# Optimization experiments

Measured on AMD Instinct MI355X. Metric: run time of the kernel, lower is better.

## Reference

```python
import jax, jax.numpy as jnp
import numpy as np

N_NODES = 50000
N_EDGES = 600000
HID = 128
N_CONVS = 3
N_GRAPHS = 64


def setup_inputs() -> dict:
    key = jax.random.key(0)
    ks = jax.random.split(key, 8)
    scale = 1.0 / np.sqrt(HID)  # ~xavier
    node_attr = jax.random.normal(ks[0], (N_NODES, HID), dtype=jnp.float32)
    edge_attr = jax.random.normal(ks[1], (N_EDGES, HID), dtype=jnp.float32)
    edge_index = jax.random.randint(ks[2], (2, N_EDGES), 0, N_NODES, dtype=jnp.int32)
    batch = jnp.sort(jax.random.randint(ks[3], (N_NODES,), 0, N_GRAPHS, dtype=jnp.int32))
    W1 = jax.random.normal(ks[4], (N_CONVS, HID, HID), dtype=jnp.float32) * scale
    B1 = jnp.zeros((N_CONVS, HID), dtype=jnp.float32)
    W2 = jax.random.normal(ks[5], (N_CONVS, HID, HID), dtype=jnp.float32) * scale
    B2 = jnp.zeros((N_CONVS, HID), dtype=jnp.float32)
    return {"node_attr": node_attr, "edge_attr": edge_attr, "edge_index": edge_index,
            "batch": batch, "W1": W1, "B1": B1, "W2": W2, "B2": B2,
            "num_graphs": N_GRAPHS}


def _gine_conv(x, edge_index, edge_attr, w1, b1, w2, b2, eps=0.0):
    src, dst = edge_index[0], edge_index[1]
    # message: softplus(x_j + edge_attr), gathered from source nodes
    msg = jax.nn.softplus(x[src] + edge_attr)          # [E, H]
    agg = jax.ops.segment_sum(msg, dst, num_segments=x.shape[0])  # [N, H]
    out = agg + (1.0 + eps) * x
    # MLP: Linear -> softplus -> Linear (torch Linear: y = x @ W.T + b)
    h = jax.nn.softplus(out @ w1.T + b1)
    return h @ w2.T + b2


def reference(node_attr, edge_attr, edge_index, batch, W1, B1, W2, B2, num_graphs):
    x = node_attr
    for i in range(N_CONVS):
        h = _gine_conv(x, edge_index, edge_attr, W1[i], B1[i], W2[i], B2[i])
        if i < N_CONVS - 1:
            h = jax.nn.softplus(h)  # inter-layer activation
        x = h
    node_feature = x
    graph_feature = jax.ops.segment_sum(node_feature, batch, num_segments=num_graphs)
    return graph_feature, node_feature
```

## Files before the change

### kernel.cpp

```cpp
#include <hip/hip_runtime.h>
#include <math.h>

#define N_NODES 50000
#define N_EDGES 600000
#define HID 128
#define N_GRAPHS 64
#define BCAP 32
#define OVF_CAP 4096
#define PCHUNK 8

typedef __attribute__((ext_vector_type(8))) short short8;
typedef __attribute__((ext_vector_type(4))) float floatx4;

__device__ __forceinline__ float softplus_f(float v) {
    return fmaxf(v, 0.0f) + __logf(1.0f + __expf(-fabsf(v)));
}

__device__ __forceinline__ float4 sp4(float4 a, float4 b) {
    return make_float4(softplus_f(a.x + b.x), softplus_f(a.y + b.y),
                       softplus_f(a.z + b.z), softplus_f(a.w + b.w));
}

__device__ __forceinline__ unsigned short f2bf(float f) {
    unsigned u = __float_as_uint(f);
    u = (u + 0x7FFFu + ((u >> 16) & 1u)) >> 16;
    return (unsigned short)u;
}

__global__ void build_buckets(const int* __restrict__ ei, int* __restrict__ cnt,
                              int2* __restrict__ bkt, int* __restrict__ ovf) {
    int e = blockIdx.x * 256 + threadIdx.x;
    if (e >= N_EDGES) return;
    int src = ei[e];
    int dst = ei[N_EDGES + e];
    int slot = atomicAdd(&cnt[dst], 1);
    if (slot < BCAP) {
        bkt[(size_t)dst * BCAP + slot] = make_int2(e, src);
    } else {
        int k = atomicAdd(&cnt[N_NODES], 1);
        if (k < OVF_CAP) ovf[k] = e;
    }
}

__global__ void __launch_bounds__(256) agg_kernel(const float* __restrict__ x,
        const float* __restrict__ edge_attr, const int* __restrict__ cnt,
        const int2* __restrict__ bkt, float* __restrict__ out) {
    int wave = blockIdx.x * 4 + (threadIdx.x >> 6);
    int lane = threadIdx.x & 63;
    int n = __builtin_amdgcn_readfirstlane(wave);
    if (n >= N_NODES) return;
    int h = lane >> 5;
    int l = lane & 31;
    int c = cnt[n]; if (c > BCAP) c = BCAP;
    const int2* bk = bkt + (size_t)n * BCAP;
    float4 acc = make_float4(0.f, 0.f, 0.f, 0.f);
    int s = 0;
    for (; s + 4 <= c; s += 4) {
        int2 pA = bk[s + h];
        int2 pB = bk[s + 2 + h];
        float4 eA = *(const float4*)(edge_attr + (size_t)pA.x * HID + l * 4);
        float4 xA = *(const float4*)(x + (size_t)pA.y * HID + l * 4);
        float4 eB = *(const float4*)(edge_attr + (size_t)pB.x * HID + l * 4);
        float4 xB = *(const float4*)(x + (size_t)pB.y * HID + l * 4);
        float4 mA = sp4(eA, xA);
        float4 mB = sp4(eB, xB);
        acc.x += mA.x + mB.x; acc.y += mA.y + mB.y;
        acc.z += mA.z + mB.z; acc.w += mA.w + mB.w;
    }
    if (s + 2 <= c) {
        int2 p = bk[s + h];
        float4 ev = *(const float4*)(edge_attr + (size_t)p.x * HID + l * 4);
        float4 xv = *(const float4*)(x + (size_t)p.y * HID + l * 4);
        float4 m = sp4(ev, xv);
        acc.x += m.x; acc.y += m.y; acc.z += m.z; acc.w += m.w;
        s += 2;
    }
    if (s < c && h == 0) {
        int2 p = bk[s];
        float4 ev = *(const float4*)(edge_attr + (size_t)p.x * HID + l * 4);
        float4 xv = *(const float4*)(x + (size_t)p.y * HID + l * 4);
        float4 m = sp4(ev, xv);
        acc.x += m.x; acc.y += m.y; acc.z += m.z; acc.w += m.w;
    }
    acc.x += __shfl(acc.x, l + 32);
    acc.y += __shfl(acc.y, l + 32);
    acc.z += __shfl(acc.z, l + 32);
    acc.w += __shfl(acc.w, l + 32);
    if (h == 0) {
        float4 xn = *(const float4*)(x + (size_t)n * HID + l * 4);
        acc.x += xn.x; acc.y += xn.y; acc.z += xn.z; acc.w += xn.w;
        *(float4*)(out + (size_t)n * HID + l * 4) = acc;
    }
}

__global__ void ovf_kernel(const float* __restrict__ x,
                           const float* __restrict__ edge_attr,
                           const int* __restrict__ ei,
                           const int* __restrict__ cnt,
                           const int* __restrict__ ovf,
                           float* __restrict__ out) {
    int lane = threadIdx.x & 63;
    int wid = threadIdx.x >> 6;
    int total = cnt[N_NODES]; if (total > OVF_CAP) total = OVF_CAP;
    for (int i = wid; i < total; i += 4) {
        int e = ovf[i];
        int src = ei[e];
        int dst = ei[N_EDGES + e];
        const float2* er = (const float2*)(edge_attr + (size_t)e * HID);
        const float2* sr = (const float2*)(x + (size_t)src * HID);
        float2 ev = er[lane];
        float2 sv = sr[lane];
        float* ap = out + (size_t)dst * HID + lane * 2;
        unsafeAtomicAdd(ap,     softplus_f(ev.x + sv.x));
        unsafeAtomicAdd(ap + 1, softplus_f(ev.y + sv.y));
    }
}

__global__ void pack_w(const float* __restrict__ W1, const float* __restrict__ W2,
                       unsigned short* __restrict__ pw) {
    int t = blockIdx.x * 256 + threadIdx.x;
    if (t >= 6 * 32 * 64) return;
    int lane = t & 63;
    int tile = (t >> 6) & 31;
    int mat = t >> 11;
    int kt = tile >> 3, nt = tile & 7;
    const float* W = (mat & 1) ? W2 : W1;
    W += (size_t)(mat >> 1) * HID * HID;
    int n = nt * 16 + (lane & 15);
    int kbase = kt * 32 + (lane >> 4) * 8;
    short8 v;
    #pragma unroll
    for (int j = 0; j < 8; j++) v[j] = (short)f2bf(W[(size_t)n * HID + kbase + j]);
    *((short8*)(pw + (size_t)t * 8)) = v;
}

__global__ void __launch_bounds__(256) mlp_mfma(const float* __restrict__ A,
        const unsigned short* __restrict__ pw, const float* __restrict__ bias,
        float* __restrict__ out, int act) {
    int wave = threadIdx.x >> 6, lane = threadIdx.x & 63;
    int r0 = (blockIdx.x * 2 + (wave >> 1)) * 16;
    int ch = wave & 1;
    int m = lane & 15, q = lane >> 4;
    int row = r0 + m;
    bool rv = row < N_NODES;
    floatx4 zero = {0.f, 0.f, 0.f, 0.f};
    floatx4 acc[4];
    #pragma unroll
    for (int t = 0; t < 4; t++) acc[t] = zero;
    const float* arow = A + (size_t)row * HID + q * 8;
    const short8* wbase = (const short8*)pw;
    #pragma unroll
    for (int kt = 0; kt < 4; kt++) {
        short8 af = {0, 0, 0, 0, 0, 0, 0, 0};
        if (rv) {
            float4 f0 = *(const float4*)(arow + kt * 32);
            float4 f1 = *(const float4*)(arow + kt * 32 + 4);
            af[0] = (short)f2bf(f0.x); af[1] = (short)f2bf(f0.y);
            af[2] = (short)f2bf(f0.z); af[3] = (short)f2bf(f0.w);
            af[4] = (short)f2bf(f1.x); af[5] = (short)f2bf(f1.y);
            af[6] = (short)f2bf(f1.z); af[7] = (short)f2bf(f1.w);
        }
        const short8* wp = wbase + (size_t)(kt * 8 + ch * 4) * 64 + lane;
        #pragma unroll
        for (int t = 0; t < 4; t++) {
            short8 bf = wp[t * 64];
            acc[t] = __builtin_amdgcn_mfma_f32_16x16x32_bf16(af, bf, acc[t], 0, 0, 0);
        }
    }
    #pragma unroll
    for (int t = 0; t < 4; t++) {
        int col = (ch * 4 + t) * 16 + m;
        float b = bias[col];
        #pragma unroll
        for (int i = 0; i < 4; i++) {
            int r = r0 + q * 4 + i;
            if (r < N_NODES) {
                float v = acc[t][i] + b;
                if (act) v = softplus_f(v);
                out[(size_t)r * HID + col] = v;
            }
        }
    }
}

__global__ void find_bounds(const int* __restrict__ batch, int* __restrict__ start) {
    int n = blockIdx.x * 256 + threadIdx.x;
    if (n >= N_NODES) return;
    int bn = batch[n];
    int bp = (n == 0) ? -1 : batch[n - 1];
    for (int g = bp + 1; g <= bn; g++) start[g] = n;
    if (n == N_NODES - 1)
        for (int g = bn + 1; g <= N_GRAPHS; g++) start[g] = N_NODES;
}

__global__ void pool_partial(const float* __restrict__ nf, const int* __restrict__ start,
                             float* __restrict__ part) {
    int g = blockIdx.x >> 3, c = blockIdx.x & (PCHUNK - 1);
    int j = threadIdx.x;
    int s = start[g], e = start[g + 1];
    int len = e - s;
    int b0 = s + (len * c) / PCHUNK;
    int b1 = s + (len * (c + 1)) / PCHUNK;
    float acc = 0.f;
    for (int n = b0; n < b1; n++) acc += nf[(size_t)n * HID + j];
    part[(size_t)blockIdx.x * HID + j] = acc;
}

__global__ void pool_final(const float* __restrict__ part, float* __restrict__ gout) {
    int g = blockIdx.x, j = threadIdx.x;
    float acc = 0.f;
    #pragma unroll
    for (int c = 0; c < PCHUNK; c++) acc += part[(size_t)(g * PCHUNK + c) * HID + j];
    gout[(size_t)g * HID + j] = acc;
}

extern "C" void kernel_launch(void* const* d_in, const int* in_sizes, int n_in,
                              void* d_out, int out_size, void* d_ws, size_t ws_size,
                              hipStream_t stream) {
    const float* node_attr = (const float*)d_in[0];
    const float* edge_attr = (const float*)d_in[1];
    const int*   ei        = (const int*)d_in[2];
    const int*   batch     = (const int*)d_in[3];
    const float* W1        = (const float*)d_in[4];
    const float* B1        = (const float*)d_in[5];
    const float* W2        = (const float*)d_in[6];
    const float* B2        = (const float*)d_in[7];

    float* gout    = (float*)d_out;
    float* nodeout = (float*)d_out + N_GRAPHS * HID;

    const size_t NH = (size_t)N_NODES * HID;
    float* P   = (float*)d_ws;
    float* Q   = P + NH;
    int*   cnt = (int*)(Q + NH);
    int*   ovf = cnt + 50002;
    int2*  bkt = (int2*)(ovf + OVF_CAP);
    unsigned short* pw = (unsigned short*)(bkt + (size_t)N_NODES * BCAP);
    int*   startb = (int*)(pw + 6 * 16384);
    float* part = (float*)(startb + 66);

    hipMemsetAsync(cnt, 0, (size_t)50001 * sizeof(int), stream);
    build_buckets<<<(N_EDGES + 255) / 256, 256, 0, stream>>>(ei, cnt, bkt, ovf);
    pack_w<<<(6 * 32 * 64 + 255) / 256, 256, 0, stream>>>(W1, W2, pw);
    find_bounds<<<(N_NODES + 255) / 256, 256, 0, stream>>>(batch, startb);

    const int agg_blocks = (N_NODES + 3) / 4;
    const int mlp_blocks = (N_NODES + 31) / 32;

    const float* xcur = node_attr;
    float* bufA = P;
    float* bufB = Q;
    for (int i = 0; i < 3; i++) {
        agg_kernel<<<agg_blocks, 256, 0, stream>>>(xcur, edge_attr, cnt, bkt, bufA);
        ovf_kernel<<<1, 256, 0, stream>>>(xcur, edge_attr, ei, cnt, ovf, bufA);
        mlp_mfma<<<mlp_blocks, 256, 0, stream>>>(bufA, pw + (size_t)(i * 2) * 16384,
                B1 + (size_t)i * HID, bufB, 1);
        float* xnext = (i == 2) ? nodeout : bufA;
        mlp_mfma<<<mlp_blocks, 256, 0, stream>>>(bufB, pw + (size_t)(i * 2 + 1) * 16384,
                B2 + (size_t)i * HID, xnext, (i < 2) ? 1 : 0);
        xcur = xnext;
        float* t = bufA; bufA = bufB; bufB = t;
    }
    pool_partial<<<N_GRAPHS * PCHUNK, HID, 0, stream>>>(nodeout, startb, part);
    pool_final<<<N_GRAPHS, HID, 0, stream>>>(part, gout);
}
```

Baseline: 839.6 us.

## Store node features in bf16, fuse MLP layers, fold overflow into aggregation

Node features and aggregated outputs are now kept in bf16 between layers, which halves the bytes of the random gathers of x[src] in the aggregation kernel. The two MLP linears are fused into one kernel, with the hidden activation staged in LDS, so the fp32 intermediate no longer makes a round trip through global memory. The separate overflow-atomic kernel is removed: nodes with more than 32 incoming edges scan the overflow list inside the aggregation kernel, which saves launches. The cost is extra bf16 rounding of the intermediates and a linear scan of the overflow list for high-degree nodes.

```diff
diff --git a/kernel.cpp b/kernel.cpp
--- a/kernel.cpp
+++ b/kernel.cpp
@@ -8,6 +8,7 @@
 #define BCAP 32
 #define OVF_CAP 4096
 #define PCHUNK 8
+#define LDSP 136
 
 typedef __attribute__((ext_vector_type(8))) short short8;
 typedef __attribute__((ext_vector_type(4))) float floatx4;
@@ -15,20 +16,25 @@
 __device__ __forceinline__ float softplus_f(float v) {
     return fmaxf(v, 0.0f) + __logf(1.0f + __expf(-fabsf(v)));
 }
-
-__device__ __forceinline__ float4 sp4(float4 a, float4 b) {
-    return make_float4(softplus_f(a.x + b.x), softplus_f(a.y + b.y),
-                       softplus_f(a.z + b.z), softplus_f(a.w + b.w));
-}
-
 __device__ __forceinline__ unsigned short f2bf(float f) {
     unsigned u = __float_as_uint(f);
     u = (u + 0x7FFFu + ((u >> 16) & 1u)) >> 16;
     return (unsigned short)u;
 }
+__device__ __forceinline__ float bflo(unsigned u) { return __uint_as_float(u << 16); }
+__device__ __forceinline__ float bfhi(unsigned u) { return __uint_as_float(u & 0xFFFF0000u); }
+
+__global__ void pack_x(const float* __restrict__ xf, unsigned short* __restrict__ xb, int nelem4) {
+    int t = blockIdx.x * 256 + threadIdx.x;
+    if (t >= nelem4) return;
+    float4 v = *(const float4*)(xf + (size_t)t * 4);
+    unsigned o0 = (unsigned)f2bf(v.x) | ((unsigned)f2bf(v.y) << 16);
+    unsigned o1 = (unsigned)f2bf(v.z) | ((unsigned)f2bf(v.w) << 16);
+    *(uint2*)(xb + (size_t)t * 4) = make_uint2(o0, o1);
+}
 
 __global__ void build_buckets(const int* __restrict__ ei, int* __restrict__ cnt,
-                              int2* __restrict__ bkt, int* __restrict__ ovf) {
+                              int2* __restrict__ bkt, int4* __restrict__ ovf) {
     int e = blockIdx.x * 256 + threadIdx.x;
     if (e >= N_EDGES) return;
     int src = ei[e];
@@ -38,20 +44,22 @@
         bkt[(size_t)dst * BCAP + slot] = make_int2(e, src);
     } else {
         int k = atomicAdd(&cnt[N_NODES], 1);
-        if (k < OVF_CAP) ovf[k] = e;
-    }
-}
-
-__global__ void __launch_bounds__(256) agg_kernel(const float* __restrict__ x,
+        if (k < OVF_CAP) ovf[k] = make_int4(e, src, dst, 0);
+    }
+}
+
+__global__ void __launch_bounds__(256) agg_kernel(const unsigned short* __restrict__ xb,
         const float* __restrict__ edge_attr, const int* __restrict__ cnt,
-        const int2* __restrict__ bkt, float* __restrict__ out) {
+        const int2* __restrict__ bkt, const int4* __restrict__ ovf,
+        unsigned short* __restrict__ outb) {
     int wave = blockIdx.x * 4 + (threadIdx.x >> 6);
     int lane = threadIdx.x & 63;
     int n = __builtin_amdgcn_readfirstlane(wave);
     if (n >= N_NODES) return;
     int h = lane >> 5;
     int l = lane & 31;
-    int c = cnt[n]; if (c > BCAP) c = BCAP;
+    int ctot = cnt[n];
+    int c = ctot < BCAP ? ctot : BCAP;
     const int2* bk = bkt + (size_t)n * BCAP;
     float4 acc = make_float4(0.f, 0.f, 0.f, 0.f);
     int s = 0;
@@ -59,60 +67,58 @@
         int2 pA = bk[s + h];
         int2 pB = bk[s + 2 + h];
         float4 eA = *(const float4*)(edge_attr + (size_t)pA.x * HID + l * 4);
-        float4 xA = *(const float4*)(x + (size_t)pA.y * HID + l * 4);
+        uint2  xA = *(const uint2*)(xb + (size_t)pA.y * HID + l * 4);
         float4 eB = *(const float4*)(edge_attr + (size_t)pB.x * HID + l * 4);
-        float4 xB = *(const float4*)(x + (size_t)pB.y * HID + l * 4);
-        float4 mA = sp4(eA, xA);
-        float4 mB = sp4(eB, xB);
-        acc.x += mA.x + mB.x; acc.y += mA.y + mB.y;
-        acc.z += mA.z + mB.z; acc.w += mA.w + mB.w;
+        uint2  xB = *(const uint2*)(xb + (size_t)pB.y * HID + l * 4);
+        acc.x += softplus_f(eA.x + bflo(xA.x)) + softplus_f(eB.x + bflo(xB.x));
+        acc.y += softplus_f(eA.y + bfhi(xA.x)) + softplus_f(eB.y + bfhi(xB.x));
+        acc.z += softplus_f(eA.z + bflo(xA.y)) + softplus_f(eB.z + bflo(xB.y));
+        acc.w += softplus_f(eA.w + bfhi(xA.y)) + softplus_f(eB.w + bfhi(xB.y));
     }
     if (s + 2 <= c) {
         int2 p = bk[s + h];
         float4 ev = *(const float4*)(edge_attr + (size_t)p.x * HID + l * 4);
-        float4 xv = *(const float4*)(x + (size_t)p.y * HID + l * 4);
-        float4 m = sp4(ev, xv);
-        acc.x += m.x; acc.y += m.y; acc.z += m.z; acc.w += m.w;
+        uint2  xv = *(const uint2*)(xb + (size_t)p.y * HID + l * 4);
+        acc.x += softplus_f(ev.x + bflo(xv.x));
+        acc.y += softplus_f(ev.y + bfhi(xv.x));
+        acc.z += softplus_f(ev.z + bflo(xv.y));
+        acc.w += softplus_f(ev.w + bfhi(xv.y));
         s += 2;
     }
     if (s < c && h == 0) {
         int2 p = bk[s];
         float4 ev = *(const float4*)(edge_attr + (size_t)p.x * HID + l * 4);
-        float4 xv = *(const float4*)(x + (size_t)p.y * HID + l * 4);
-        float4 m = sp4(ev, xv);
-        acc.x += m.x; acc.y += m.y; acc.z += m.z; acc.w += m.w;
+        uint2  xv = *(const uint2*)(xb + (size_t)p.y * HID + l * 4);
+        acc.x += softplus_f(ev.x + bflo(xv.x));
+        acc.y += softplus_f(ev.y + bfhi(xv.x));
+        acc.z += softplus_f(ev.z + bflo(xv.y));
+        acc.w += softplus_f(ev.w + bfhi(xv.y));
+    }
+    if (ctot > BCAP) {
+        int k = cnt[N_NODES]; if (k > OVF_CAP) k = OVF_CAP;
+        for (int i = 0; i < k; i++) {
+            int4 t = ovf[i];
+            if (t.z == n && h == 0) {
+                float4 ev = *(const float4*)(edge_attr + (size_t)t.x * HID + l * 4);
+                uint2  xv = *(const uint2*)(xb + (size_t)t.y * HID + l * 4);
+                acc.x += softplus_f(ev.x + bflo(xv.x));
+                acc.y += softplus_f(ev.y + bfhi(xv.x));
+                acc.z += softplus_f(ev.z + bflo(xv.y));
+                acc.w += softplus_f(ev.w + bfhi(xv.y));
+            }
+        }
     }
     acc.x += __shfl(acc.x, l + 32);
     acc.y += __shfl(acc.y, l + 32);
     acc.z += __shfl(acc.z, l + 32);
     acc.w += __shfl(acc.w, l + 32);
     if (h == 0) {
-        float4 xn = *(const float4*)(x + (size_t)n * HID + l * 4);
-        acc.x += xn.x; acc.y += xn.y; acc.z += xn.z; acc.w += xn.w;
-        *(float4*)(out + (size_t)n * HID + l * 4) = acc;
-    }
-}
-
-__global__ void ovf_kernel(const float* __restrict__ x,
-                           const float* __restrict__ edge_attr,
-                           const int* __restrict__ ei,
-                           const int* __restrict__ cnt,
-                           const int* __restrict__ ovf,
-                           float* __restrict__ out) {
-    int lane = threadIdx.x & 63;
-    int wid = threadIdx.x >> 6;
-    int total = cnt[N_NODES]; if (total > OVF_CAP) total = OVF_CAP;
-    for (int i = wid; i < total; i += 4) {
-        int e = ovf[i];
-        int src = ei[e];
-        int dst = ei[N_EDGES + e];
-        const float2* er = (const float2*)(edge_attr + (size_t)e * HID);
-        const float2* sr = (const float2*)(x + (size_t)src * HID);
-        float2 ev = er[lane];
-        float2 sv = sr[lane];
-        float* ap = out + (size_t)dst * HID + lane * 2;
-        unsafeAtomicAdd(ap,     softplus_f(ev.x + sv.x));
-        unsafeAtomicAdd(ap + 1, softplus_f(ev.y + sv.y));
+        uint2 xn = *(const uint2*)(xb + (size_t)n * HID + l * 4);
+        acc.x += bflo(xn.x); acc.y += bfhi(xn.x);
+        acc.z += bflo(xn.y); acc.w += bfhi(xn.y);
+        unsigned o0 = (unsigned)f2bf(acc.x) | ((unsigned)f2bf(acc.y) << 16);
+        unsigned o1 = (unsigned)f2bf(acc.z) | ((unsigned)f2bf(acc.w) << 16);
+        *(uint2*)(outb + (size_t)n * HID + l * 4) = make_uint2(o0, o1);
     }
 }
 
@@ -134,51 +140,84 @@
     *((short8*)(pw + (size_t)t * 8)) = v;
 }
 
-__global__ void __launch_bounds__(256) mlp_mfma(const float* __restrict__ A,
-        const unsigned short* __restrict__ pw, const float* __restrict__ bias,
-        float* __restrict__ out, int act) {
+__global__ void __launch_bounds__(256) mlp_fused(const unsigned short* __restrict__ A,
+        const unsigned short* __restrict__ pw1, const unsigned short* __restrict__ pw2,
+        const float* __restrict__ b1, const float* __restrict__ b2,
+        void* __restrict__ outp, int final_layer) {
+    __shared__ __align__(16) unsigned short hl[2][16][LDSP];
     int wave = threadIdx.x >> 6, lane = threadIdx.x & 63;
-    int r0 = (blockIdx.x * 2 + (wave >> 1)) * 16;
-    int ch = wave & 1;
+    int rt = wave >> 1, ch = wave & 1;
     int m = lane & 15, q = lane >> 4;
+    int r0 = blockIdx.x * 32 + rt * 16;
     int row = r0 + m;
     bool rv = row < N_NODES;
+    short8 zf = {0, 0, 0, 0, 0, 0, 0, 0};
     floatx4 zero = {0.f, 0.f, 0.f, 0.f};
     floatx4 acc[4];
     #pragma unroll
     for (int t = 0; t < 4; t++) acc[t] = zero;
-    const float* arow = A + (size_t)row * HID + q * 8;
-    const short8* wbase = (const short8*)pw;
+    const short8* ar = (const short8*)(A + (size_t)row * HID + q * 8);
+    const short8* w1 = (const short8*)pw1;
     #pragma unroll
     for (int kt = 0; kt < 4; kt++) {
-        short8 af = {0, 0, 0, 0, 0, 0, 0, 0};
-        if (rv) {
-            float4 f0 = *(const float4*)(arow + kt * 32);
-            float4 f1 = *(const float4*)(arow + kt * 32 + 4);
-            af[0] = (short)f2bf(f0.x); af[1] = (short)f2bf(f0.y);
-            af[2] = (short)f2bf(f0.z); af[3] = (short)f2bf(f0.w);
-            af[4] = (short)f2bf(f1.x); af[5] = (short)f2bf(f1.y);
-            af[6] = (short)f2bf(f1.z); af[7] = (short)f2bf(f1.w);
+        short8 af = rv ? ar[kt * 4] : zf;
+        const short8* wp = w1 + (size_t)(kt * 8 + ch * 4) * 64 + lane;
+        #pragma unroll
+        for (int t = 0; t < 4; t++)
+            acc[t] = __builtin_amdgcn_mfma_f32_16x16x32_bf16(af, wp[t * 64], acc[t], 0, 0, 0);
+    }
+    #pragma unroll
+    for (int t = 0; t < 4; t++) {
+        int col = ch * 64 + t * 16 + m;
+        float bb = b1[col];
+        #pragma unroll
+        for (int i = 0; i < 4; i++)
+            hl[rt][q * 4 + i][col] = f2bf(softplus_f(acc[t][i] + bb));
+    }
+    __syncthreads();
+    #pragma unroll
+    for (int t = 0; t < 4; t++) acc[t] = zero;
+    const short8* w2 = (const short8*)pw2;
+    #pragma unroll
+    for (int kt = 0; kt < 4; kt++) {
+        short8 af = *(const short8*)&hl[rt][m][kt * 32 + q * 8];
+        const short8* wp = w2 + (size_t)(kt * 8 + ch * 4) * 64 + lane;
+        #pragma unroll
+        for (int t = 0; t < 4; t++)
+            acc[t] = __builtin_amdgcn_mfma_f32_16x16x32_bf16(af, wp[t * 64], acc[t], 0, 0, 0);
+    }
+    if (final_layer) {
+        float* out = (float*)outp;
+        #pragma unroll
+        for (int t = 0; t < 4; t++) {
+            int col = ch * 64 + t * 16 + m;
+            float bb = b2[col];
+            #pragma unroll
+            for (int i = 0; i < 4; i++) {
+                int r = r0 + q * 4 + i;
+                if (r < N_NODES) out[(size_t)r * HID + col] = acc[t][i] + bb;
+            }
         }
-        const short8* wp = wbase + (size_t)(kt * 8 + ch * 4) * 64 + lane;
+    } else {
+        __syncthreads();
         #pragma unroll
         for (int t = 0; t < 4; t++) {
-            short8 bf = wp[t * 64];
-            acc[t] = __builtin_amdgcn_mfma_f32_16x16x32_bf16(af, bf, acc[t], 0, 0, 0);
+            int col = ch * 64 + t * 16 + m;
+            float bb = b2[col];
+            #pragma unroll
+            for (int i = 0; i < 4; i++)
+                hl[rt][q * 4 + i][col] = f2bf(softplus_f(acc[t][i] + bb));
         }
-    }
-    #pragma unroll
-    for (int t = 0; t < 4; t++) {
-        int col = (ch * 4 + t) * 16 + m;
-        float b = bias[col];
-        #pragma unroll
-        for (int i = 0; i < 4; i++) {
-            int r = r0 + q * 4 + i;
-            if (r < N_NODES) {
-                float v = acc[t][i] + b;
-                if (act) v = softplus_f(v);
-                out[(size_t)r * HID + col] = v;
-            }
+        __syncthreads();
+        unsigned short* outb = (unsigned short*)outp;
+        int tid = threadIdx.x;
+        int orow = tid >> 3, cseg = (tid & 7) * 16;
+        int gr = blockIdx.x * 32 + orow;
+        if (gr < N_NODES) {
+            uint4 v0 = *(const uint4*)&hl[orow >> 4][orow & 15][cseg];
+            uint4 v1 = *(const uint4*)&hl[orow >> 4][orow & 15][cseg + 8];
+            *(uint4*)(outb + (size_t)gr * HID + cseg) = v0;
+            *(uint4*)(outb + (size_t)gr * HID + cseg + 8) = v1;
         }
     }
 }
@@ -230,36 +269,33 @@
     float* nodeout = (float*)d_out + N_GRAPHS * HID;
 
     const size_t NH = (size_t)N_NODES * HID;
-    float* P   = (float*)d_ws;
-    float* Q   = P + NH;
-    int*   cnt = (int*)(Q + NH);
-    int*   ovf = cnt + 50002;
+    unsigned short* nab  = (unsigned short*)d_ws;
+    unsigned short* bufA = nab + NH;
+    unsigned short* bufB = bufA + NH;
+    int*   cnt = (int*)(bufB + NH);
+    int4*  ovf = (int4*)(cnt + 50004);
     int2*  bkt = (int2*)(ovf + OVF_CAP);
     unsigned short* pw = (unsigned short*)(bkt + (size_t)N_NODES * BCAP);
     int*   startb = (int*)(pw + 6 * 16384);
-    float* part = (float*)(startb + 66);
+    float* part = (float*)(startb + 68);
 
     hipMemsetAsync(cnt, 0, (size_t)50001 * sizeof(int), stream);
     build_buckets<<<(N_EDGES + 255) / 256, 256, 0, stream>>>(ei, cnt, bkt, ovf);
     pack_w<<<(6 * 32 * 64 + 255) / 256, 256, 0, stream>>>(W1, W2, pw);
+    pack_x<<<((int)(NH / 4) + 255) / 256, 256, 0, stream>>>(node_attr, nab, (int)(NH / 4));
     find_bounds<<<(N_NODES + 255) / 256, 256, 0, stream>>>(batch, startb);
 
     const int agg_blocks = (N_NODES + 3) / 4;
     const int mlp_blocks = (N_NODES + 31) / 32;
 
-    const float* xcur = node_attr;
-    float* bufA = P;
-    float* bufB = Q;
+    const unsigned short* xcur = nab;
     for (int i = 0; i < 3; i++) {
-        agg_kernel<<<agg_blocks, 256, 0, stream>>>(xcur, edge_attr, cnt, bkt, bufA);
-        ovf_kernel<<<1, 256, 0, stream>>>(xcur, edge_attr, ei, cnt, ovf, bufA);
-        mlp_mfma<<<mlp_blocks, 256, 0, stream>>>(bufA, pw + (size_t)(i * 2) * 16384,
-                B1 + (size_t)i * HID, bufB, 1);
-        float* xnext = (i == 2) ? nodeout : bufA;
-        mlp_mfma<<<mlp_blocks, 256, 0, stream>>>(bufB, pw + (size_t)(i * 2 + 1) * 16384,
-                B2 + (size_t)i * HID, xnext, (i < 2) ? 1 : 0);
-        xcur = xnext;
-        float* t = bufA; bufA = bufB; bufB = t;
+        agg_kernel<<<agg_blocks, 256, 0, stream>>>(xcur, edge_attr, cnt, bkt, ovf, bufA);
+        void* outp = (i == 2) ? (void*)nodeout : (void*)bufB;
+        mlp_fused<<<mlp_blocks, 256, 0, stream>>>(bufA,
+                pw + (size_t)(i * 2) * 16384, pw + (size_t)(i * 2 + 1) * 16384,
+                B1 + (size_t)i * HID, B2 + (size_t)i * HID, outp, (i == 2) ? 1 : 0);
+        xcur = bufB;
     }
     pool_partial<<<N_GRAPHS * PCHUNK, HID, 0, stream>>>(nodeout, startb, part);
     pool_final<<<N_GRAPHS, HID, 0, stream>>>(part, gout);
```

Result: faster. 745.4 us (-11.2%).
